# Performance work log

Measured on AMD Instinct MI355X. Metric: run time of the kernel, lower is better.

The kernel has to match this reference:

```python
import jax, jax.numpy as jnp
import numpy as np

N = 4096; B = 32; LATENT = 16; UNITS = 64; NNZ = 65536; K = 2; M = 2 * K + 1

def _spmm(rows, cols, vals, x):
    # sparse [N,N] @ dense [N,FB] via gather + segment_sum
    return jax.ops.segment_sum(vals[:, None] * x[cols], rows, num_segments=N)

def _gconv(y, supports, W, b):
    # y: (B, N*F) -> Chebyshev-style diffusion over each support, then dense projection
    F = y.shape[1] // N
    x0 = y.reshape(B, N, F).transpose(1, 2, 0).reshape(N, F * B)
    xs = [x0]
    for rows, cols, vals in supports:
        x1 = _spmm(rows, cols, vals, x0)
        xs.append(x1)
        xk1, xk2 = x1, x0
        for _ in range(2, K + 1):
            x2 = 2.0 * _spmm(rows, cols, vals, xk1) - xk2
            xs.append(x2)
            xk1, xk2 = x2, xk1
    # [M,N,F,B] -> [B,N,F,M] -> [B*N, F*M], matching torch permute/reshape
    x = jnp.stack(xs).reshape(M, N, F, B).transpose(3, 1, 2, 0).reshape(B * N, F * M)
    return (x @ W + b).reshape(B, N * W.shape[1])

def setup_inputs():
    key = jax.random.key(0)
    ks = jax.random.split(key, 8)
    r = jax.random.randint(ks[0], (NNZ,), 0, N)
    c = jax.random.randint(ks[1], (NNZ,), 0, N)
    v = jax.random.uniform(ks[2], (NNZ,)) + 0.1
    d_row = jax.ops.segment_sum(v, r, num_segments=N)
    d_col = jax.ops.segment_sum(v, c, num_segments=N)
    inv_row = jnp.where(d_row > 0, 1.0 / d_row, 0.0)
    inv_col = jnp.where(d_col > 0, 1.0 / d_col, 0.0)
    # support1 = (D_out^{-1} A)^T ; support2 = (D_in^{-1} A^T)^T  (COO triples)
    s1_rows, s1_cols, s1_vals = c, r, v * inv_row[r]
    s2_rows, s2_cols, s2_vals = r, c, v * inv_col[c]
    def xavier(k, shape):
        scale = np.sqrt(2.0 / (shape[0] + shape[1])).astype(np.float32)
        return jax.random.normal(k, shape, dtype=jnp.float32) * scale
    return {
        "t_local": 0,
        "y": jax.random.normal(ks[3], (B, N * LATENT), dtype=jnp.float32),
        "W_theta": xavier(ks[4], (LATENT * M, LATENT)),
        "b_lat": jnp.ones((LATENT,), jnp.float32),  # bias_start=1.0; shared (LayerParams keys biases by length)
        "W_hid": xavier(ks[5], (LATENT * M, UNITS)),
        "b_hid": jnp.zeros((UNITS,), jnp.float32),
        "W_out": xavier(ks[6], (UNITS * M, LATENT)),
        "s1_rows": s1_rows, "s1_cols": s1_cols, "s1_vals": s1_vals,
        "s2_rows": s2_rows, "s2_cols": s2_cols, "s2_vals": s2_vals,
    }

def reference(t_local, y, W_theta, b_lat, W_hid, b_hid, W_out,
              s1_rows, s1_cols, s1_vals, s2_rows, s2_cols, s2_vals):
    supports = [(s1_rows, s1_cols, s1_vals), (s2_rows, s2_cols, s2_vals)]
    theta = jax.nn.sigmoid(_gconv(y, supports, W_theta, b_lat))
    c = jnp.tanh(_gconv(y, supports, W_hid, b_hid))   # gen_layers = 1
    c = jnp.tanh(_gconv(c, supports, W_out, b_lat))   # shared bias of length latent_dim
    return -theta * c
```

## Files before the change

kernel.cpp:

```cpp
#include <hip/hip_runtime.h>
#include <stdint.h>

#define NN    4096
#define BB    32
#define NNZE  65536
#define WA    512
#define WB    2048
#define WD    512

typedef __attribute__((ext_vector_type(8))) short bf16x8;
typedef __attribute__((ext_vector_type(4))) float f32x4;

__device__ __forceinline__ float bf2f_lo(unsigned int u) {
    union { unsigned int x; float f; } c; c.x = u << 16; return c.f;
}
__device__ __forceinline__ float bf2f_hi(unsigned int u) {
    union { unsigned int x; float f; } c; c.x = u & 0xffff0000u; return c.f;
}
__device__ __forceinline__ float bf2f(unsigned int h) {
    union { unsigned int u; float f; } c; c.u = h << 16; return c.f;
}
__device__ __forceinline__ unsigned int f2bf(float f) {
    union { float ff; unsigned int u; } c; c.ff = f;
    return (c.u + 0x7fffu + ((c.u >> 16) & 1u)) >> 16;
}

__global__ void hist2_kernel(const int* __restrict__ r1, const int* __restrict__ r2,
                             int* __restrict__ cnt1, int* __restrict__ cnt2) {
    int e = blockIdx.x * blockDim.x + threadIdx.x;
    if (e < NNZE) atomicAdd(&cnt1[r1[e]], 1);
    else          atomicAdd(&cnt2[r2[e - NNZE]], 1);
}

__global__ void scan2_kernel(int* cur1, int* rp1, int* cur2, int* rp2) {
    int* cur = (blockIdx.x == 0) ? cur1 : cur2;
    int* rp  = (blockIdx.x == 0) ? rp1  : rp2;
    __shared__ int part[256];
    int t = threadIdx.x;
    int base = t * 16;
    int loc[16];
    int s = 0;
#pragma unroll
    for (int i = 0; i < 16; ++i) { loc[i] = s; s += cur[base + i]; }
    part[t] = s;
    __syncthreads();
    for (int off = 1; off < 256; off <<= 1) {
        int v = 0;
        if (t >= off) v = part[t - off];
        __syncthreads();
        part[t] += v;
        __syncthreads();
    }
    int excl = (t == 0) ? 0 : part[t - 1];
#pragma unroll
    for (int i = 0; i < 16; ++i) rp[base + i] = excl + loc[i];
    __syncthreads();
#pragma unroll
    for (int i = 0; i < 16; ++i) cur[base + i] = rp[base + i];
    if (t == 255) rp[4096] = part[255];
}

__global__ void scatter2_kernel(const int* __restrict__ r1, const int* __restrict__ c1, const float* __restrict__ v1,
                                const int* __restrict__ r2, const int* __restrict__ c2, const float* __restrict__ v2,
                                int* __restrict__ cur1, int* __restrict__ cur2,
                                int2* __restrict__ ep1, int2* __restrict__ ep2) {
    int e = blockIdx.x * blockDim.x + threadIdx.x;
    if (e < NNZE) {
        int pos = atomicAdd(&cur1[r1[e]], 1);
        ep1[pos] = make_int2(c1[e], __float_as_int(v1[e]));
    } else {
        int ee = e - NNZE;
        int pos = atomicAdd(&cur2[r2[ee]], 1);
        ep2[pos] = make_int2(c2[ee], __float_as_int(v2[ee]));
    }
}

__global__ void transA_kernel(const float* __restrict__ y, unsigned short* __restrict__ x0h) {
    int t = threadIdx.x, n = blockIdx.x;
    int b = t & 31, q = t >> 5;
    float4 y4 = *(const float4*)(y + (size_t)b * (NN * 16) + n * 16 + 4 * q);
    uint2 o;
    o.x = f2bf(y4.x) | (f2bf(y4.y) << 16);
    o.y = f2bf(y4.z) | (f2bf(y4.w) << 16);
    *(uint2*)(x0h + (size_t)n * WA + b * 16 + 4 * q) = o;
}

struct SpmmDesc {
    const unsigned short* in;
    const unsigned short* prev;
    float* outF;
    unsigned short* outH;
    const int* rp; const int2* ep;
    float alpha, beta;
};

__device__ __forceinline__ void gather_row(const unsigned short* __restrict__ in,
                                           const int* __restrict__ rp, const int2* __restrict__ ep,
                                           int row, int t, float* acc) {
    int beg = rp[row], end = rp[row + 1];
    for (int i0 = beg; i0 < end; i0 += 64) {
        int nn = end - i0; if (nn > 64) nn = 64;
        int2 epr = make_int2(0, 0);
        if (i0 + t < end) epr = ep[i0 + t];
        int vcol = epr.x, vvb = epr.y;
#pragma unroll 4
        for (int j = 0; j < nn; ++j) {
            int sc = __builtin_amdgcn_readlane(vcol, j);
            float v = __int_as_float(__builtin_amdgcn_readlane(vvb, j));
            const uint4* xr = (const uint4*)(in + (size_t)sc * WD);
            uint4 xv = xr[t];
            acc[0] += v * bf2f_lo(xv.x); acc[1] += v * bf2f_hi(xv.x);
            acc[2] += v * bf2f_lo(xv.y); acc[3] += v * bf2f_hi(xv.y);
            acc[4] += v * bf2f_lo(xv.z); acc[5] += v * bf2f_hi(xv.z);
            acc[6] += v * bf2f_lo(xv.w); acc[7] += v * bf2f_hi(xv.w);
        }
    }
}

__launch_bounds__(64)
__global__ void spmmD_kernel(SpmmDesc q0, SpmmDesc q1, SpmmDesc q2, SpmmDesc q3, int ninst) {
    int blk = blockIdx.x;
    int xcd = blk & 7;
    int idx = blk >> 3;
    int spx = 8 / ninst;
    int inst = xcd / spx;
    int sub  = xcd - inst * spx;
    int row  = sub * (NN / spx) + idx;
    SpmmDesc q = (inst == 0) ? q0 : (inst == 1) ? q1 : (inst == 2) ? q2 : q3;
    int t = threadIdx.x;
    float acc[8];
#pragma unroll
    for (int k = 0; k < 8; ++k) acc[k] = 0.f;
    gather_row(q.in, q.rp, q.ep, row, t, acc);
    float r[8];
#pragma unroll
    for (int k = 0; k < 8; ++k) r[k] = q.alpha * acc[k];
    if (q.prev) {
        uint4 pv = ((const uint4*)(q.prev + (size_t)row * WD))[t];
        r[0] += q.beta * bf2f_lo(pv.x); r[1] += q.beta * bf2f_hi(pv.x);
        r[2] += q.beta * bf2f_lo(pv.y); r[3] += q.beta * bf2f_hi(pv.y);
        r[4] += q.beta * bf2f_lo(pv.z); r[5] += q.beta * bf2f_hi(pv.z);
        r[6] += q.beta * bf2f_lo(pv.w); r[7] += q.beta * bf2f_hi(pv.w);
    }
    if (q.outF) {
        float* po = q.outF + (size_t)row * WD + t * 8;
        *(float4*)(po)     = make_float4(r[0], r[1], r[2], r[3]);
        *(float4*)(po + 4) = make_float4(r[4], r[5], r[6], r[7]);
    } else {
        uint4 o;
        o.x = f2bf(r[0]) | (f2bf(r[1]) << 16);
        o.y = f2bf(r[2]) | (f2bf(r[3]) << 16);
        o.z = f2bf(r[4]) | (f2bf(r[5]) << 16);
        o.w = f2bf(r[6]) | (f2bf(r[7]) << 16);
        ((uint4*)(q.outH + (size_t)row * WD))[t] = o;
    }
}

__launch_bounds__(256)
__global__ void projA_mfma(const unsigned short* __restrict__ xh,
                           const float* __restrict__ Wtheta, const float* __restrict__ Whid,
                           const float* __restrict__ b_hid,
                           float* __restrict__ theta,
                           unsigned short* __restrict__ c) {
    __shared__ __align__(16) unsigned short sW[80 * 104];
    int t = threadIdx.x;
    for (int i = t; i < 80 * 96; i += 256) {
        int col = i / 96, k = i - col * 96;
        int m = k >> 4, f = k & 15;
        float v = 0.f;
        if (m < 5) v = (col < 16) ? Wtheta[(f * 5 + m) * 16 + col]
                                  : Whid[(f * 5 + m) * 64 + (col - 16)];
        sW[col * 104 + k] = (unsigned short)f2bf(v);
    }
    __syncthreads();
    int lane = t & 63, w = t >> 6;
    int r = lane & 15, g = lane >> 4;
    bf16x8 wf[5][3];
#pragma unroll
    for (int ct = 0; ct < 5; ++ct)
#pragma unroll
        for (int kt = 0; kt < 3; ++kt)
            wf[ct][kt] = *(const bf16x8*)(sW + (ct * 16 + r) * 104 + kt * 32 + g * 8);
    float bh[4];
#pragma unroll
    for (int ct = 0; ct < 4; ++ct) bh[ct] = b_hid[ct * 16 + r];

    for (int i = 0; i < 2; ++i) {
        int n = blockIdx.x * 8 + w * 2 + i;
        f32x4 acc[2][5];
#pragma unroll
        for (int bt = 0; bt < 2; ++bt)
#pragma unroll
            for (int ct = 0; ct < 5; ++ct)
                acc[bt][ct] = (f32x4){0.f, 0.f, 0.f, 0.f};
#pragma unroll
        for (int kt = 0; kt < 3; ++kt) {
            bf16x8 a[2];
            int m = kt * 2 + (g >> 1);
#pragma unroll
            for (int bt = 0; bt < 2; ++bt) {
                bf16x8 av = {0, 0, 0, 0, 0, 0, 0, 0};
                if (m < 5)
                    av = *(const bf16x8*)(xh + ((size_t)m * NN + n) * WA
                                          + (bt * 16 + r) * 16 + (g & 1) * 8);
                a[bt] = av;
            }
#pragma unroll
            for (int bt = 0; bt < 2; ++bt)
#pragma unroll
                for (int ct = 0; ct < 5; ++ct)
                    acc[bt][ct] = __builtin_amdgcn_mfma_f32_16x16x32_bf16(
                        a[bt], wf[ct][kt], acc[bt][ct], 0, 0, 0);
        }
#pragma unroll
        for (int bt = 0; bt < 2; ++bt) {
#pragma unroll
            for (int reg = 0; reg < 4; ++reg) {
                int b = bt * 16 + g * 4 + reg;
                theta[(size_t)n * 512 + b * 16 + r] = acc[bt][0][reg];
            }
#pragma unroll
            for (int ct = 1; ct < 5; ++ct) {
                int u = (ct - 1) * 16 + r;
#pragma unroll
                for (int reg = 0; reg < 4; ++reg) {
                    int b = bt * 16 + g * 4 + reg;
                    float hv = tanhf(acc[bt][ct][reg] + bh[ct - 1]);
                    c[(size_t)n * WB + b * 64 + u] = (unsigned short)f2bf(hv);
                }
            }
        }
    }
}

__launch_bounds__(256)
__global__ void preproj_mfma(const unsigned short* __restrict__ c,
                             const float* __restrict__ Wout,
                             float* __restrict__ d0,
                             unsigned short* __restrict__ dd1, unsigned short* __restrict__ dd2,
                             unsigned short* __restrict__ dd3, unsigned short* __restrict__ dd4) {
    __shared__ __align__(16) unsigned short sW[80 * 72];
    int t = threadIdx.x;
    for (int i = t; i < 80 * 64; i += 256) {
        int col = i >> 6, k = i & 63;
        int m = col >> 4, up = col & 15;
        sW[col * 72 + k] = (unsigned short)f2bf(Wout[(k * 5 + m) * 16 + up]);
    }
    __syncthreads();
    int lane = t & 63, w = t >> 6;
    int r = lane & 15, g = lane >> 4;
    bf16x8 wf[5][2];
#pragma unroll
    for (int ct = 0; ct < 5; ++ct)
#pragma unroll
        for (int kt = 0; kt < 2; ++kt)
            wf[ct][kt] = *(const bf16x8*)(sW + (ct * 16 + r) * 72 + kt * 32 + g * 8);

    for (int i = 0; i < 2; ++i) {
        int n = blockIdx.x * 8 + w * 2 + i;
        f32x4 acc[2][5];
#pragma unroll
        for (int bt = 0; bt < 2; ++bt)
#pragma unroll
            for (int ct = 0; ct < 5; ++ct)
                acc[bt][ct] = (f32x4){0.f, 0.f, 0.f, 0.f};
#pragma unroll
        for (int kt = 0; kt < 2; ++kt) {
            bf16x8 a[2];
#pragma unroll
            for (int bt = 0; bt < 2; ++bt)
                a[bt] = *(const bf16x8*)(c + (size_t)n * WB + (bt * 16 + r) * 64
                                         + kt * 32 + g * 8);
#pragma unroll
            for (int bt = 0; bt < 2; ++bt)
#pragma unroll
                for (int ct = 0; ct < 5; ++ct)
                    acc[bt][ct] = __builtin_amdgcn_mfma_f32_16x16x32_bf16(
                        a[bt], wf[ct][kt], acc[bt][ct], 0, 0, 0);
        }
#pragma unroll
        for (int bt = 0; bt < 2; ++bt) {
#pragma unroll
            for (int reg = 0; reg < 4; ++reg) {
                int b = bt * 16 + g * 4 + reg;
                d0[(size_t)n * WD + b * 16 + r] = acc[bt][0][reg];
            }
#pragma unroll
            for (int ct = 1; ct < 5; ++ct) {
                unsigned short* dp = (ct == 1) ? dd1 : (ct == 2) ? dd2 : (ct == 3) ? dd3 : dd4;
#pragma unroll
                for (int reg = 0; reg < 4; ++reg) {
                    int b = bt * 16 + g * 4 + reg;
                    dp[(size_t)n * WD + b * 16 + r] = (unsigned short)f2bf(acc[bt][ct][reg]);
                }
            }
        }
    }
}

__launch_bounds__(64)
__global__ void finalspmm_kernel(const unsigned short* __restrict__ g1, const unsigned short* __restrict__ g3,
                                 const int* __restrict__ rp1, const int2* __restrict__ ep1,
                                 const int* __restrict__ rp2, const int2* __restrict__ ep2,
                                 const float* __restrict__ theta, const float* __restrict__ d0,
                                 const unsigned short* __restrict__ dd2, const unsigned short* __restrict__ dd4,
                                 const float* __restrict__ b_lat, float* __restrict__ out) {
    int blk = blockIdx.x;
    int row = (blk & 7) * 512 + (blk >> 3);
    int t = threadIdx.x;
    float h[8];
#pragma unroll
    for (int k = 0; k < 8; ++k) h[k] = 0.f;
    gather_row(g1, rp1, ep1, row, t, h);
    gather_row(g3, rp2, ep2, row, t, h);
    size_t base = (size_t)row * WD + t * 8;
    float4 dA = *(const float4*)(d0 + base);
    float4 dB = *(const float4*)(d0 + base + 4);
    uint4 p2 = *(const uint4*)(dd2 + base);
    uint4 p4 = *(const uint4*)(dd4 + base);
    float4 tA = *(const float4*)(theta + base);
    float4 tB = *(const float4*)(theta + base + 4);
    float4 blA = *(const float4*)(b_lat + (t & 1) * 8);
    float4 blB = *(const float4*)(b_lat + (t & 1) * 8 + 4);
    float tot[8], th[8];
    tot[0] = dA.x - bf2f_lo(p2.x) - bf2f_lo(p4.x) + h[0] + blA.x;
    tot[1] = dA.y - bf2f_hi(p2.x) - bf2f_hi(p4.x) + h[1] + blA.y;
    tot[2] = dA.z - bf2f_lo(p2.y) - bf2f_lo(p4.y) + h[2] + blA.z;
    tot[3] = dA.w - bf2f_hi(p2.y) - bf2f_hi(p4.y) + h[3] + blA.w;
    tot[4] = dB.x - bf2f_lo(p2.z) - bf2f_lo(p4.z) + h[4] + blB.x;
    tot[5] = dB.y - bf2f_hi(p2.z) - bf2f_hi(p4.z) + h[5] + blB.y;
    tot[6] = dB.z - bf2f_lo(p2.w) - bf2f_lo(p4.w) + h[6] + blB.z;
    tot[7] = dB.w - bf2f_hi(p2.w) - bf2f_hi(p4.w) + h[7] + blB.w;
    th[0] = tA.x + blA.x; th[1] = tA.y + blA.y; th[2] = tA.z + blA.z; th[3] = tA.w + blA.w;
    th[4] = tB.x + blB.x; th[5] = tB.y + blB.y; th[6] = tB.z + blB.z; th[7] = tB.w + blB.w;
    float res[8];
#pragma unroll
    for (int j = 0; j < 8; ++j)
        res[j] = -(1.f / (1.f + expf(-th[j]))) * tanhf(tot[j]);
    float* po = out + ((size_t)(t >> 1) * NN + row) * 16 + (t & 1) * 8;
    *(float4*)(po)     = make_float4(res[0], res[1], res[2], res[3]);
    *(float4*)(po + 4) = make_float4(res[4], res[5], res[6], res[7]);
}

extern "C" void kernel_launch(void* const* d_in, const int* in_sizes, int n_in,
                              void* d_out, int out_size, void* d_ws, size_t ws_size,
                              hipStream_t stream) {
    const float* y      = (const float*)d_in[1];
    const float* Wtheta = (const float*)d_in[2];
    const float* b_lat  = (const float*)d_in[3];
    const float* Whid   = (const float*)d_in[4];
    const float* b_hid  = (const float*)d_in[5];
    const float* Wout   = (const float*)d_in[6];
    const int*   r1     = (const int*)d_in[7];
    const int*   c1     = (const int*)d_in[8];
    const float* v1     = (const float*)d_in[9];
    const int*   r2     = (const int*)d_in[10];
    const int*   c2     = (const int*)d_in[11];
    const float* v2     = (const float*)d_in[12];
    float* out = (float*)d_out;

    char* ws = (char*)d_ws;
    size_t off = 0;
    auto alloc = [&](size_t bytes) -> char* {
        char* p = ws + off;
        off += (bytes + 255) & ~(size_t)255;
        return p;
    };
    int*   rp1   = (int*)alloc(4097 * 4);
    int*   rp2   = (int*)alloc(4097 * 4);
    int*   cur1  = (int*)alloc(4096 * 4);
    int*   cur2  = (int*)alloc(4096 * 4);
    int2*  ep1   = (int2*)alloc((size_t)NNZE * 8);
    int2*  ep2   = (int2*)alloc((size_t)NNZE * 8);
    unsigned short* xh = (unsigned short*)alloc((size_t)5 * NN * WA * 2);
    float* theta = (float*)alloc((size_t)NN * 512 * 4);
    char*  creg  = alloc((size_t)NN * WB * 2);
    float* d0 = (float*)alloc((size_t)NN * WD * 4);
    unsigned short* g1 = (unsigned short*)alloc((size_t)NN * WD * 2);
    unsigned short* g3 = (unsigned short*)alloc((size_t)NN * WD * 2);
    if (off > ws_size) return;

    unsigned short* x0h = xh;
    unsigned short* x1h = xh + (size_t)1 * NN * WA;
    unsigned short* x2h = xh + (size_t)2 * NN * WA;
    unsigned short* x3h = xh + (size_t)3 * NN * WA;
    unsigned short* x4h = xh + (size_t)4 * NN * WA;
    unsigned short* cbuf = (unsigned short*)creg;
    unsigned short* dd1 = (unsigned short*)((char*)xh + ((size_t)0  << 20));
    unsigned short* dd2 = (unsigned short*)((char*)xh + ((size_t)4  << 20));
    unsigned short* dd3 = (unsigned short*)((char*)xh + ((size_t)8  << 20));
    unsigned short* dd4 = (unsigned short*)((char*)xh + ((size_t)12 << 20));

    hipMemsetAsync(cur1, 0, 2 * 4096 * 4, stream);
    hist2_kernel<<<2 * NNZE / 256, 256, 0, stream>>>(r1, r2, cur1, cur2);
    scan2_kernel<<<2, 256, 0, stream>>>(cur1, rp1, cur2, rp2);
    scatter2_kernel<<<2 * NNZE / 256, 256, 0, stream>>>(r1, c1, v1, r2, c2, v2,
                                                        cur1, cur2, ep1, ep2);

    transA_kernel<<<NN, 128, 0, stream>>>(y, x0h);
    {
        SpmmDesc a0 = { x0h, nullptr, nullptr, x1h, rp1, ep1, 1.f, 0.f };
        SpmmDesc a1 = { x0h, nullptr, nullptr, x3h, rp2, ep2, 1.f, 0.f };
        spmmD_kernel<<<2 * NN, 64, 0, stream>>>(a0, a1, a0, a1, 2);
    }
    {
        SpmmDesc a0 = { x1h, x0h, nullptr, x2h, rp1, ep1, 2.f, -1.f };
        SpmmDesc a1 = { x3h, x0h, nullptr, x4h, rp2, ep2, 2.f, -1.f };
        spmmD_kernel<<<2 * NN, 64, 0, stream>>>(a0, a1, a0, a1, 2);
    }
    projA_mfma<<<NN / 8, 256, 0, stream>>>(xh, Wtheta, Whid, b_hid, theta, cbuf);

    preproj_mfma<<<NN / 8, 256, 0, stream>>>(cbuf, Wout, d0, dd1, dd2, dd3, dd4);
    {
        SpmmDesc a0 = { dd2, dd1, nullptr, g1, rp1, ep1, 2.f, 1.f };
        SpmmDesc a1 = { dd4, dd3, nullptr, g3, rp2, ep2, 2.f, 1.f };
        spmmD_kernel<<<2 * NN, 64, 0, stream>>>(a0, a1, a0, a1, 2);
    }
    finalspmm_kernel<<<NN, 64, 0, stream>>>(g1, g3, rp1, ep1, rp2, ep2,
                                            theta, d0, dd2, dd4, b_lat, out);
}
```

Baseline: 222.7 us.

## Fuse projection kernels via LDS hidden state and stage edge lists in LDS

```diff
diff --git a/kernel.cpp b/kernel.cpp
--- a/kernel.cpp
+++ b/kernel.cpp
@@ -5,7 +5,6 @@
 #define BB    32
 #define NNZE  65536
 #define WA    512
-#define WB    2048
 #define WD    512
 
 typedef __attribute__((ext_vector_type(8))) short bf16x8;
@@ -94,21 +93,20 @@
     float alpha, beta;
 };
 
-__device__ __forceinline__ void gather_row(const unsigned short* __restrict__ in,
-                                           const int* __restrict__ rp, const int2* __restrict__ ep,
-                                           int row, int t, float* acc) {
+__device__ __forceinline__ void gather_row_lds(const unsigned short* __restrict__ in,
+                                               const int* __restrict__ rp, const int2* __restrict__ ep,
+                                               int row, int t, int* scol, float* sval, float* acc) {
     int beg = rp[row], end = rp[row + 1];
     for (int i0 = beg; i0 < end; i0 += 64) {
         int nn = end - i0; if (nn > 64) nn = 64;
-        int2 epr = make_int2(0, 0);
-        if (i0 + t < end) epr = ep[i0 + t];
-        int vcol = epr.x, vvb = epr.y;
+        __syncthreads();
+        if (t < nn) { int2 e = ep[i0 + t]; scol[t] = e.x; sval[t] = __int_as_float(e.y); }
+        __syncthreads();
 #pragma unroll 4
         for (int j = 0; j < nn; ++j) {
-            int sc = __builtin_amdgcn_readlane(vcol, j);
-            float v = __int_as_float(__builtin_amdgcn_readlane(vvb, j));
-            const uint4* xr = (const uint4*)(in + (size_t)sc * WD);
+            const uint4* xr = (const uint4*)(in + (size_t)scol[j] * WD);
             uint4 xv = xr[t];
+            float v = sval[j];
             acc[0] += v * bf2f_lo(xv.x); acc[1] += v * bf2f_hi(xv.x);
             acc[2] += v * bf2f_lo(xv.y); acc[3] += v * bf2f_hi(xv.y);
             acc[4] += v * bf2f_lo(xv.z); acc[5] += v * bf2f_hi(xv.z);
@@ -119,6 +117,8 @@
 
 __launch_bounds__(64)
 __global__ void spmmD_kernel(SpmmDesc q0, SpmmDesc q1, SpmmDesc q2, SpmmDesc q3, int ninst) {
+    __shared__ int scol[64];
+    __shared__ float sval[64];
     int blk = blockIdx.x;
     int xcd = blk & 7;
     int idx = blk >> 3;
@@ -131,7 +131,7 @@
     float acc[8];
 #pragma unroll
     for (int k = 0; k < 8; ++k) acc[k] = 0.f;
-    gather_row(q.in, q.rp, q.ep, row, t, acc);
+    gather_row_lds(q.in, q.rp, q.ep, row, t, scol, sval, acc);
     float r[8];
 #pragma unroll
     for (int k = 0; k < 8; ++k) r[k] = q.alpha * acc[k];
@@ -157,12 +157,16 @@
 }
 
 __launch_bounds__(256)
-__global__ void projA_mfma(const unsigned short* __restrict__ xh,
+__global__ void proj_fused(const unsigned short* __restrict__ xh,
                            const float* __restrict__ Wtheta, const float* __restrict__ Whid,
-                           const float* __restrict__ b_hid,
+                           const float* __restrict__ b_hid, const float* __restrict__ Wout,
                            float* __restrict__ theta,
-                           unsigned short* __restrict__ c) {
-    __shared__ __align__(16) unsigned short sW[80 * 104];
+                           float* __restrict__ d0,
+                           unsigned short* __restrict__ dd1, unsigned short* __restrict__ dd2,
+                           unsigned short* __restrict__ dd3, unsigned short* __restrict__ dd4) {
+    __shared__ __align__(16) unsigned short sWa[80 * 104];
+    __shared__ __align__(16) unsigned short sWo[80 * 72];
+    __shared__ __align__(16) unsigned short sC[4][32 * 72];
     int t = threadIdx.x;
     for (int i = t; i < 80 * 96; i += 256) {
         int col = i / 96, k = i - col * 96;
@@ -170,20 +174,26 @@
         float v = 0.f;
         if (m < 5) v = (col < 16) ? Wtheta[(f * 5 + m) * 16 + col]
                                   : Whid[(f * 5 + m) * 64 + (col - 16)];
-        sW[col * 104 + k] = (unsigned short)f2bf(v);
+        sWa[col * 104 + k] = (unsigned short)f2bf(v);
+    }
+    for (int i = t; i < 80 * 64; i += 256) {
+        int col = i >> 6, k = i & 63;
+        int m = col >> 4, up = col & 15;
+        sWo[col * 72 + k] = (unsigned short)f2bf(Wout[(k * 5 + m) * 16 + up]);
     }
     __syncthreads();
     int lane = t & 63, w = t >> 6;
     int r = lane & 15, g = lane >> 4;
-    bf16x8 wf[5][3];
+    bf16x8 wfa[5][3];
 #pragma unroll
     for (int ct = 0; ct < 5; ++ct)
 #pragma unroll
         for (int kt = 0; kt < 3; ++kt)
-            wf[ct][kt] = *(const bf16x8*)(sW + (ct * 16 + r) * 104 + kt * 32 + g * 8);
+            wfa[ct][kt] = *(const bf16x8*)(sWa + (ct * 16 + r) * 104 + kt * 32 + g * 8);
     float bh[4];
 #pragma unroll
     for (int ct = 0; ct < 4; ++ct) bh[ct] = b_hid[ct * 16 + r];
+    unsigned short* myC = (unsigned short*)sC[w];
 
     for (int i = 0; i < 2; ++i) {
         int n = blockIdx.x * 8 + w * 2 + i;
@@ -210,7 +220,7 @@
 #pragma unroll
                 for (int ct = 0; ct < 5; ++ct)
                     acc[bt][ct] = __builtin_amdgcn_mfma_f32_16x16x32_bf16(
-                        a[bt], wf[ct][kt], acc[bt][ct], 0, 0, 0);
+                        a[bt], wfa[ct][kt], acc[bt][ct], 0, 0, 0);
         }
 #pragma unroll
         for (int bt = 0; bt < 2; ++bt) {
@@ -225,65 +235,37 @@
 #pragma unroll
                 for (int reg = 0; reg < 4; ++reg) {
                     int b = bt * 16 + g * 4 + reg;
-                    float hv = tanhf(acc[bt][ct][reg] + bh[ct - 1]);
-                    c[(size_t)n * WB + b * 64 + u] = (unsigned short)f2bf(hv);
+                    myC[b * 72 + u] = (unsigned short)f2bf(tanhf(acc[bt][ct][reg] + bh[ct - 1]));
                 }
             }
         }
-    }
-}
-
-__launch_bounds__(256)
-__global__ void preproj_mfma(const unsigned short* __restrict__ c,
-                             const float* __restrict__ Wout,
-                             float* __restrict__ d0,
-                             unsigned short* __restrict__ dd1, unsigned short* __restrict__ dd2,
-                             unsigned short* __restrict__ dd3, unsigned short* __restrict__ dd4) {
-    __shared__ __align__(16) unsigned short sW[80 * 72];
-    int t = threadIdx.x;
-    for (int i = t; i < 80 * 64; i += 256) {
-        int col = i >> 6, k = i & 63;
-        int m = col >> 4, up = col & 15;
-        sW[col * 72 + k] = (unsigned short)f2bf(Wout[(k * 5 + m) * 16 + up]);
-    }
-    __syncthreads();
-    int lane = t & 63, w = t >> 6;
-    int r = lane & 15, g = lane >> 4;
-    bf16x8 wf[5][2];
-#pragma unroll
-    for (int ct = 0; ct < 5; ++ct)
-#pragma unroll
-        for (int kt = 0; kt < 2; ++kt)
-            wf[ct][kt] = *(const bf16x8*)(sW + (ct * 16 + r) * 72 + kt * 32 + g * 8);
-
-    for (int i = 0; i < 2; ++i) {
-        int n = blockIdx.x * 8 + w * 2 + i;
-        f32x4 acc[2][5];
+        f32x4 acc2[2][5];
 #pragma unroll
         for (int bt = 0; bt < 2; ++bt)
 #pragma unroll
             for (int ct = 0; ct < 5; ++ct)
-                acc[bt][ct] = (f32x4){0.f, 0.f, 0.f, 0.f};
+                acc2[bt][ct] = (f32x4){0.f, 0.f, 0.f, 0.f};
 #pragma unroll
         for (int kt = 0; kt < 2; ++kt) {
-            bf16x8 a[2];
+            bf16x8 a2[2];
 #pragma unroll
             for (int bt = 0; bt < 2; ++bt)
-                a[bt] = *(const bf16x8*)(c + (size_t)n * WB + (bt * 16 + r) * 64
-                                         + kt * 32 + g * 8);
-#pragma unroll
-            for (int bt = 0; bt < 2; ++bt)
-#pragma unroll
-                for (int ct = 0; ct < 5; ++ct)
-                    acc[bt][ct] = __builtin_amdgcn_mfma_f32_16x16x32_bf16(
-                        a[bt], wf[ct][kt], acc[bt][ct], 0, 0, 0);
+                a2[bt] = *(const bf16x8*)(myC + (bt * 16 + r) * 72 + kt * 32 + g * 8);
+#pragma unroll
+            for (int ct = 0; ct < 5; ++ct) {
+                bf16x8 wo = *(const bf16x8*)(sWo + (ct * 16 + r) * 72 + kt * 32 + g * 8);
+#pragma unroll
+                for (int bt = 0; bt < 2; ++bt)
+                    acc2[bt][ct] = __builtin_amdgcn_mfma_f32_16x16x32_bf16(
+                        a2[bt], wo, acc2[bt][ct], 0, 0, 0);
+            }
         }
 #pragma unroll
         for (int bt = 0; bt < 2; ++bt) {
 #pragma unroll
             for (int reg = 0; reg < 4; ++reg) {
                 int b = bt * 16 + g * 4 + reg;
-                d0[(size_t)n * WD + b * 16 + r] = acc[bt][0][reg];
+                d0[(size_t)n * WD + b * 16 + r] = acc2[bt][0][reg];
             }
 #pragma unroll
             for (int ct = 1; ct < 5; ++ct) {
@@ -291,7 +273,7 @@
 #pragma unroll
                 for (int reg = 0; reg < 4; ++reg) {
                     int b = bt * 16 + g * 4 + reg;
-                    dp[(size_t)n * WD + b * 16 + r] = (unsigned short)f2bf(acc[bt][ct][reg]);
+                    dp[(size_t)n * WD + b * 16 + r] = (unsigned short)f2bf(acc2[bt][ct][reg]);
                 }
             }
         }
@@ -305,14 +287,16 @@
                                  const float* __restrict__ theta, const float* __restrict__ d0,
                                  const unsigned short* __restrict__ dd2, const unsigned short* __restrict__ dd4,
                                  const float* __restrict__ b_lat, float* __restrict__ out) {
+    __shared__ int scol[64];
+    __shared__ float sval[64];
     int blk = blockIdx.x;
     int row = (blk & 7) * 512 + (blk >> 3);
     int t = threadIdx.x;
     float h[8];
 #pragma unroll
     for (int k = 0; k < 8; ++k) h[k] = 0.f;
-    gather_row(g1, rp1, ep1, row, t, h);
-    gather_row(g3, rp2, ep2, row, t, h);
+    gather_row_lds(g1, rp1, ep1, row, t, scol, sval, h);
+    gather_row_lds(g3, rp2, ep2, row, t, scol, sval, h);
     size_t base = (size_t)row * WD + t * 8;
     float4 dA = *(const float4*)(d0 + base);
     float4 dB = *(const float4*)(d0 + base + 4);
@@ -374,10 +358,13 @@
     int2*  ep2   = (int2*)alloc((size_t)NNZE * 8);
     unsigned short* xh = (unsigned short*)alloc((size_t)5 * NN * WA * 2);
     float* theta = (float*)alloc((size_t)NN * 512 * 4);
-    char*  creg  = alloc((size_t)NN * WB * 2);
-    float* d0 = (float*)alloc((size_t)NN * WD * 4);
-    unsigned short* g1 = (unsigned short*)alloc((size_t)NN * WD * 2);
-    unsigned short* g3 = (unsigned short*)alloc((size_t)NN * WD * 2);
+    float* d0    = (float*)alloc((size_t)NN * WD * 4);
+    unsigned short* dd1 = (unsigned short*)alloc((size_t)NN * WD * 2);
+    unsigned short* dd2 = (unsigned short*)alloc((size_t)NN * WD * 2);
+    unsigned short* dd3 = (unsigned short*)alloc((size_t)NN * WD * 2);
+    unsigned short* dd4 = (unsigned short*)alloc((size_t)NN * WD * 2);
+    unsigned short* g1  = (unsigned short*)alloc((size_t)NN * WD * 2);
+    unsigned short* g3  = (unsigned short*)alloc((size_t)NN * WD * 2);
     if (off > ws_size) return;
 
     unsigned short* x0h = xh;
@@ -385,11 +372,6 @@
     unsigned short* x2h = xh + (size_t)2 * NN * WA;
     unsigned short* x3h = xh + (size_t)3 * NN * WA;
     unsigned short* x4h = xh + (size_t)4 * NN * WA;
-    unsigned short* cbuf = (unsigned short*)creg;
-    unsigned short* dd1 = (unsigned short*)((char*)xh + ((size_t)0  << 20));
-    unsigned short* dd2 = (unsigned short*)((char*)xh + ((size_t)4  << 20));
-    unsigned short* dd3 = (unsigned short*)((char*)xh + ((size_t)8  << 20));
-    unsigned short* dd4 = (unsigned short*)((char*)xh + ((size_t)12 << 20));
 
     hipMemsetAsync(cur1, 0, 2 * 4096 * 4, stream);
     hist2_kernel<<<2 * NNZE / 256, 256, 0, stream>>>(r1, r2, cur1, cur2);
@@ -408,9 +390,10 @@
         SpmmDesc a1 = { x3h, x0h, nullptr, x4h, rp2, ep2, 2.f, -1.f };
         spmmD_kernel<<<2 * NN, 64, 0, stream>>>(a0, a1, a0, a1, 2);
     }
-    projA_mfma<<<NN / 8, 256, 0, stream>>>(xh, Wtheta, Whid, b_hid, theta, cbuf);
-
-    preproj_mfma<<<NN / 8, 256, 0, stream>>>(cbuf, Wout, d0, dd1, dd2, dd3, dd4);
+
+    proj_fused<<<NN / 8, 256, 0, stream>>>(xh, Wtheta, Whid, b_hid, Wout,
+                                           theta, d0, dd1, dd2, dd3, dd4);
+
     {
         SpmmDesc a0 = { dd2, dd1, nullptr, g1, rp1, ep1, 2.f, 1.f };
         SpmmDesc a1 = { dd4, dd3, nullptr, g3, rp2, ep2, 2.f, 1.f };
```

Measured after the change: 199.4 us. 10.5% less time.
